# Performance work log

Measured on AMD Instinct MI355X. Metric: run time of the kernel, lower is better.

The kernel has to match this reference:

```python
import jax, jax.numpy as jnp
import numpy as np

N = 100000      # num_edges in original graph = nodes here
E = 1600000     # edges of the line-graph
F_IN = 16       # num_edge_features
H, C = 2, 32    # heads, hidden_channels
HC = H * C
TD = 16         # time_embedding_dim
CD = 16         # condition_dim
NC = 2          # num_classes
MAX_TIME = 1000.0
THETA = 1.0


def _glorot(key, shape):
    fan_in = shape[0]
    return jax.random.normal(key, shape, dtype=jnp.float32) / np.sqrt(fan_in)


def setup_inputs() -> dict:
    key = jax.random.key(0)
    ks = jax.random.split(key, 32)
    inp = {
        "x": jax.random.normal(ks[0], (N, F_IN), dtype=jnp.float32),
        "edge_index": jax.random.randint(ks[1], (2, E), 0, N, dtype=jnp.int64),
        "t": jax.random.randint(ks[2], (1,), 0, 1000, dtype=jnp.int64),
        "condition": jax.random.normal(ks[3], (N, CD), dtype=jnp.float32),
        # GATv2 layer 0 (bias=True)
        "Wl0": _glorot(ks[4], (F_IN, HC)), "bl0": jnp.zeros((HC,), jnp.float32),
        "Wr0": _glorot(ks[5], (F_IN, HC)), "br0": jnp.zeros((HC,), jnp.float32),
        "att0": _glorot(ks[6], (H, C)), "bias0": jnp.zeros((HC,), jnp.float32),
        "Wres0": _glorot(ks[7], (F_IN, HC)), "bres0": jnp.zeros((HC,), jnp.float32),
        # GATv2 layer 1 (bias=False)
        "Wl1": _glorot(ks[8], (HC, HC)),
        "Wr1": _glorot(ks[9], (HC, HC)),
        "att1": _glorot(ks[10], (H, C)),
        "Wres1": _glorot(ks[11], (HC, HC)), "bres1": jnp.zeros((HC,), jnp.float32),
        # time MLP
        "Wt0": _glorot(ks[12], (TD, TD)), "bt0": jnp.zeros((TD,), jnp.float32),
        "Wt1": _glorot(ks[13], (TD, TD)), "bt1": jnp.zeros((TD,), jnp.float32),
        # decoder heads
        "Wfd": _glorot(ks[14], (HC + CD + TD, C)), "bfd": jnp.zeros((C,), jnp.float32),
        "Wcls": _glorot(ks[15], (C, NC)), "bcls": jnp.zeros((NC,), jnp.float32),
    }
    return inp


def _segment_softmax(logits, seg, num_seg):
    # logits: [E, H], softmax over edges sharing the same destination node
    m = jax.ops.segment_max(logits, seg, num_segments=num_seg)
    ex = jnp.exp(logits - m[seg])
    s = jax.ops.segment_sum(ex, seg, num_segments=num_seg)
    return ex / (s[seg] + 1e-16)


def _gatv2(x, src, dst, Wl, bl, Wr, br, att, bias):
    # PyG GATv2Conv with add_self_loops (self loops appended by caller)
    xl = x @ Wl
    xr = x @ Wr
    if bl is not None:
        xl = xl + bl
        xr = xr + br
    xl = xl.reshape(-1, H, C)
    xr = xr.reshape(-1, H, C)
    e = jax.nn.leaky_relu(xl[src] + xr[dst], negative_slope=0.2)  # [E, H, C]
    logits = jnp.einsum('ehc,hc->eh', e, att)                     # [E, H]
    alpha = _segment_softmax(logits, dst, N)                      # [E, H]
    msg = xl[src] * alpha[:, :, None]                             # [E, H, C]
    out = jax.ops.segment_sum(msg, dst, num_segments=N)           # [N, H, C]
    out = out.reshape(N, HC)
    if bias is not None:
        out = out + bias
    return out


def _time_embedding(t):
    tf = t.astype(jnp.float32) * (1000.0 / MAX_TIME)
    half = TD // 2
    freqs = jnp.exp(jnp.arange(half, dtype=jnp.float32) * -(jnp.log(10000.0) / (half - 1)))
    ang = tf[:, None] * freqs[None, :]
    return jnp.concatenate([jnp.sin(ang), jnp.cos(ang)], axis=1)  # [1, TD]


def reference(x, edge_index, t, condition,
              Wl0, bl0, Wr0, br0, att0, bias0, Wres0, bres0,
              Wl1, Wr1, att1, Wres1, bres1,
              Wt0, bt0, Wt1, bt1, Wfd, bfd, Wcls, bcls):
    loops = jnp.arange(N, dtype=edge_index.dtype)
    src = jnp.concatenate([edge_index[0], loops])
    dst = jnp.concatenate([edge_index[1], loops])

    # layer 0
    res = jax.nn.relu(x @ Wres0 + bres0)
    h = jax.nn.relu(_gatv2(x, src, dst, Wl0, bl0, Wr0, br0, att0, bias0))
    h = THETA * h + res
    # layer 1 (bias=False)
    res = jax.nn.relu(h @ Wres1 + bres1)
    h2 = jax.nn.relu(_gatv2(h, src, dst, Wl1, None, Wr1, None, att1, None))
    h = THETA * h2 + res

    # mode == 'future'
    t_emb = _time_embedding(t)
    t_emb = jax.nn.silu(t_emb @ Wt0 + bt0)
    t_emb = jax.nn.silu(t_emb @ Wt1 + bt1)
    t_rep = jnp.tile(t_emb, (N, 1))                                # [N, TD]
    h = jnp.concatenate([h, t_rep, condition], axis=1)             # [N, HC+TD+CD]
    logits = h @ Wfd + bfd
    logits = logits @ Wcls + bcls
    return logits[None]                                            # [1, N, NC]
```

## Files before the change

kernel.cpp:

```cpp
#include <hip/hip_runtime.h>
#include <hip/hip_bf16.h>
#include <hip/hip_fp16.h>
#include <math.h>


#define BLK 256
#define BDST 32
#define CDST 256
#define CHUNK 4096
#define FCAP 768
#define NBC_MAX 512

typedef _Float16 half4v __attribute__((ext_vector_type(4)));
typedef _Float16 half2v __attribute__((ext_vector_type(2)));

#if __has_builtin(__builtin_amdgcn_fdot2)
#define FDOT2(a, b, c) __builtin_amdgcn_fdot2((a), (b), (c), false)
#else
__device__ __forceinline__ float fdot2_fallback(half2v a, half2v b, float c) {
    return c + (float)a.x * (float)b.x + (float)a.y * (float)b.y;
}
#define FDOT2(a, b, c) fdot2_fallback((a), (b), (c))
#endif

__device__ __forceinline__ float relu(float x) { return x > 0.f ? x : 0.f; }

__device__ __forceinline__ float edot(half4v h, half2v xlo, half2v xhi,
                                      half2v alo, half2v ahi, half2v c02) {
    half2v lo = half2v{h.x, h.y} + xlo;
    half2v hi = half2v{h.z, h.w} + xhi;
    lo = __builtin_elementwise_max(lo, lo * c02);
    hi = __builtin_elementwise_max(hi, hi * c02);
    return FDOT2(lo, alo, FDOT2(hi, ahi, 0.f));
}

__global__ void k_tiny(const int* __restrict__ t,
                       const float* __restrict__ Wt0, const float* __restrict__ bt0,
                       const float* __restrict__ Wt1, const float* __restrict__ bt1,
                       const float* __restrict__ Wfd, const float* __restrict__ bfd,
                       const float* __restrict__ Wcls, const float* __restrict__ bcls,
                       const float* __restrict__ Wl1, const float* __restrict__ Wr1,
                       const float* __restrict__ Wres1,
                       float* __restrict__ wcomb,
                       float* __restrict__ bfinal,
                       half4v* __restrict__ w16,
                       int* __restrict__ ccnt, int NBC)
{
    __shared__ float temb[16];
    int tid = threadIdx.x;
    for (int i = tid; i < NBC; i += BLK) ccnt[i] = 0;
    for (int idx = tid; idx < 3 * 1024; idx += BLK) {
        int m = idx >> 10, rem = idx & 1023;
        int k4 = rem >> 6, c = rem & 63;
        const float* W = (m == 0) ? Wl1 : (m == 1) ? Wr1 : Wres1;
        half4v v;
        v.x = (_Float16)W[(4 * k4 + 0) * 64 + c];
        v.y = (_Float16)W[(4 * k4 + 1) * 64 + c];
        v.z = (_Float16)W[(4 * k4 + 2) * 64 + c];
        v.w = (_Float16)W[(4 * k4 + 3) * 64 + c];
        w16[idx] = v;
    }
    if (tid == 0) {
        float tf = (float)t[0];
        float e0[16], v1[16];
        const float cexp = -logf(10000.f) / 7.f;
        for (int j = 0; j < 8; ++j) {
            float ang = tf * expf((float)j * cexp);
            e0[j] = sinf(ang);
            e0[8 + j] = cosf(ang);
        }
        for (int i = 0; i < 16; ++i) {
            float a = bt0[i];
            for (int j = 0; j < 16; ++j) a += e0[j] * Wt0[j * 16 + i];
            v1[i] = a / (1.f + expf(-a));
        }
        for (int i = 0; i < 16; ++i) {
            float a = bt1[i];
            for (int j = 0; j < 16; ++j) a += v1[j] * Wt1[j * 16 + i];
            temb[i] = a / (1.f + expf(-a));
        }
    }
    __syncthreads();
    if (tid < 192) {
        int i = tid >> 1, k = tid & 1;
        float a = 0.f;
        for (int j = 0; j < 32; ++j) a += Wfd[i * 32 + j] * Wcls[j * 2 + k];
        wcomb[tid] = a;
    }
    __syncthreads();
    if (tid < 2) {
        float a = bcls[tid];
        for (int j = 0; j < 32; ++j) a += bfd[j] * Wcls[j * 2 + tid];
        for (int d = 0; d < 16; ++d) a += temb[d] * wcomb[(64 + d) * 2 + tid];
        bfinal[tid] = a;
    }
}

__global__ void k_histc(const int* __restrict__ ei, int E, int NBC,
                        int* __restrict__ ccnt)
{
    __shared__ int h[NBC_MAX];
    int tid = threadIdx.x;
    for (int i = tid; i < NBC; i += BLK) h[i] = 0;
    __syncthreads();
    int e0 = blockIdx.x * CHUNK;
    #pragma unroll
    for (int k = 0; k < CHUNK / BLK; ++k) {
        int e = e0 + tid + k * BLK;
        if (e < E) atomicAdd(&h[ei[E + e] >> 8], 1);
    }
    __syncthreads();
    for (int i = tid; i < NBC; i += BLK) {
        int v = h[i];
        if (v) atomicAdd(&ccnt[i], v);
    }
}

__global__ void k_scan(const int* __restrict__ ccnt, int NBC, int E,
                       int* __restrict__ cbase, int* __restrict__ ccur)
{
    if (threadIdx.x == 0) {
        int acc = 0;
        for (int i = 0; i < NBC; ++i) {
            cbase[i] = acc;
            acc += ccnt[i];
        }
        cbase[NBC] = acc;
    }
    __syncthreads();
    for (int i = threadIdx.x; i < NBC; i += BLK) ccur[i] = cbase[i];
}

__global__ void k_part(const int* __restrict__ ei, int E, int NBC,
                       int* __restrict__ ccur, int* __restrict__ part)
{
    __shared__ int h[NBC_MAX];
    __shared__ int gb[NBC_MAX];
    int tid = threadIdx.x;
    int e0 = blockIdx.x * CHUNK;
    for (int i = tid; i < NBC; i += BLK) h[i] = 0;
    __syncthreads();
    int sv[CHUNK / BLK], dv[CHUNK / BLK];
    #pragma unroll
    for (int k = 0; k < CHUNK / BLK; ++k) {
        int e = e0 + tid + k * BLK;
        if (e < E) {
            sv[k] = ei[e];
            dv[k] = ei[E + e];
            atomicAdd(&h[dv[k] >> 8], 1);
        } else dv[k] = -1;
    }
    __syncthreads();
    for (int i = tid; i < NBC; i += BLK) {
        int v = h[i];
        gb[i] = v ? atomicAdd(&ccur[i], v) : 0;
    }
    __syncthreads();
    for (int i = tid; i < NBC; i += BLK) h[i] = gb[i];
    __syncthreads();
    #pragma unroll
    for (int k = 0; k < CHUNK / BLK; ++k) {
        if (dv[k] >= 0) {
            int p = atomicAdd(&h[dv[k] >> 8], 1);
            part[p] = (sv[k] << 8) | (dv[k] & 255);
        }
    }
}

__global__ void k_refine(const int* __restrict__ cbase, const int* __restrict__ part,
                         int NBF, int* __restrict__ fbeg, int* __restrict__ fend,
                         int* __restrict__ srcs)
{
    __shared__ int fcnt[8];
    __shared__ int fcur[8];
    int b = blockIdx.x, tid = threadIdx.x;
    int beg = cbase[b], end = cbase[b + 1];
    if (tid < 8) fcnt[tid] = 0;
    __syncthreads();
    for (int k = beg + tid; k < end; k += BLK)
        atomicAdd(&fcnt[(part[k] >> 5) & 7], 1);
    __syncthreads();
    if (tid == 0) {
        int acc = beg;
        #pragma unroll
        for (int f = 0; f < 8; ++f) {
            int fb = b * 8 + f;
            fcur[f] = acc;
            if (fb < NBF) { fbeg[fb] = acc; acc += fcnt[f]; fend[fb] = acc; }
        }
    }
    __syncthreads();
    for (int k = beg + tid; k < end; k += BLK) {
        int tg = part[k];
        int p = atomicAdd(&fcur[(tg >> 5) & 7], 1);
        srcs[p] = ((tg >> 8) << 5) | (tg & 31);
    }
}

__global__ void k_pre0f(const float* __restrict__ x,
                        const float* __restrict__ Wl, const float* __restrict__ bl,
                        const float* __restrict__ Wr, const float* __restrict__ br,
                        const float* __restrict__ Wres, const float* __restrict__ bres,
                        _Float16* __restrict__ xlh, _Float16* __restrict__ xr16,
                        _Float16* __restrict__ res16, int N)
{
    int wid = (int)(((long long)blockIdx.x * BLK + threadIdx.x) >> 6);
    int lane = threadIdx.x & 63;
    int g = lane >> 4, q = lane & 15;
    int n = wid * 4 + g;
    bool valid = n < N;
    int nn = valid ? n : N - 1;
    float xv = x[(size_t)nn * 16 + q];
    int c0 = q * 4;
    float4 accl = *(const float4*)(bl + c0);
    float4 accr = *(const float4*)(br + c0);
    float4 accs = *(const float4*)(bres + c0);
    #pragma unroll
    for (int k = 0; k < 16; ++k) {
        float xk = __shfl(xv, (g << 4) | k, 64);
        float4 wl = *(const float4*)(Wl + k * 64 + c0);
        float4 wr = *(const float4*)(Wr + k * 64 + c0);
        float4 wsv = *(const float4*)(Wres + k * 64 + c0);
        accl.x = fmaf(xk, wl.x, accl.x);
        accl.y = fmaf(xk, wl.y, accl.y);
        accl.z = fmaf(xk, wl.z, accl.z);
        accl.w = fmaf(xk, wl.w, accl.w);
        accr.x = fmaf(xk, wr.x, accr.x);
        accr.y = fmaf(xk, wr.y, accr.y);
        accr.z = fmaf(xk, wr.z, accr.z);
        accr.w = fmaf(xk, wr.w, accr.w);
        accs.x = fmaf(xk, wsv.x, accs.x);
        accs.y = fmaf(xk, wsv.y, accs.y);
        accs.z = fmaf(xk, wsv.z, accs.z);
        accs.w = fmaf(xk, wsv.w, accs.w);
    }
    if (valid) {
        size_t base = (size_t)n * 64 + c0;
        half4v hl, hr, hs;
        hl.x = (_Float16)accl.x; hl.y = (_Float16)accl.y;
        hl.z = (_Float16)accl.z; hl.w = (_Float16)accl.w;
        hr.x = (_Float16)accr.x; hr.y = (_Float16)accr.y;
        hr.z = (_Float16)accr.z; hr.w = (_Float16)accr.w;
        hs.x = (_Float16)relu(accs.x); hs.y = (_Float16)relu(accs.y);
        hs.z = (_Float16)relu(accs.z); hs.w = (_Float16)relu(accs.w);
        *(half4v*)(xlh + base) = hl;
        *(half4v*)(xr16 + base) = hr;
        *(half4v*)(res16 + base) = hs;
    }
}

template <int LAYER>
__global__ void k_gat3(const int* __restrict__ fbeg, const int* __restrict__ fend,
                       const int* __restrict__ srcs,
                       const _Float16* __restrict__ xlh, const _Float16* __restrict__ xr16,
                       const float* __restrict__ att, const float* __restrict__ bias,
                       const _Float16* __restrict__ res16,
                       const half4v* __restrict__ w16, const float* __restrict__ bres1,
                       _Float16* __restrict__ xlh_out, _Float16* __restrict__ xr_out,
                       _Float16* __restrict__ res_out,
                       const float* __restrict__ cond, const float* __restrict__ wcomb,
                       const float* __restrict__ bfinal, float* __restrict__ out,
                       int N)
{
    __shared__ int lh[BDST];
    __shared__ int rp[BDST + 1];
    __shared__ int cc[BDST];
    __shared__ int sidx[BDST];
    __shared__ int tags[FCAP];
    __shared__ half4v h4[LAYER == 0 ? 32 : 1][16];

    int b = blockIdx.x;
    int tid = threadIdx.x;
    int beg = fbeg[b];
    int nE = fend[b] - beg; if (nE > FCAP) nE = FCAP;

    if (tid < BDST) lh[tid] = 0;
    __syncthreads();
    for (int k = tid; k < nE; k += BLK) atomicAdd(&lh[srcs[beg + k] & 31], 1);
    __syncthreads();
    if (tid == 0) {
        int acc = 0;
        rp[0] = 0;
        #pragma unroll
        for (int i = 0; i < BDST; ++i) { acc += lh[i]; rp[i + 1] = acc; }
    }
    __syncthreads();
    if (tid < BDST) cc[tid] = rp[tid];
    __syncthreads();
    for (int k = tid; k < nE; k += BLK) {
        int tg = srcs[beg + k];
        int r = atomicAdd(&cc[tg & 31], 1);
        tags[r] = tg >> 5;
    }
    if (tid < BDST) {
        int di = rp[tid + 1] - rp[tid];
        int r = 0;
        #pragma unroll
        for (int j = 0; j < BDST; ++j) {
            int dj = rp[j + 1] - rp[j];
            r += (dj > di) || (dj == di && j < tid);
        }
        sidx[r] = tid;
    }
    __syncthreads();

    int lane = tid & 63, w = tid >> 6;
    int g = lane >> 4, q = lane & 15;
    int c0 = q * 4;
    float4 a4f = *(const float4*)(att + c0);
    const half2v c02 = { (_Float16)0.2f, (_Float16)0.2f };
    half2v alo = { (_Float16)a4f.x, (_Float16)a4f.y };
    half2v ahi = { (_Float16)a4f.z, (_Float16)a4f.w };

    #pragma unroll
    for (int rep = 0; rep < 2; ++rep) {
        int dlow = sidx[w * 8 + rep * 4 + g];
        int node = b * BDST + dlow;
        bool nvalid = node < N;
        int n = nvalid ? node : 0;

        half4v xrh = *(const half4v*)(xr16 + (size_t)n * 64 + c0);
        half2v xlo = { xrh.x, xrh.y }, xhi = { xrh.z, xrh.w };

        half4v hsv = *(const half4v*)(xlh + (size_t)n * 64 + c0);
        float lv = edot(hsv, xlo, xhi, alo, ahi, c02);
        lv += __shfl_xor(lv, 1, 8);
        lv += __shfl_xor(lv, 2, 8);
        lv += __shfl_xor(lv, 4, 8);

        float m = lv, den = 1.f;
        float ac0 = (float)hsv.x, ac1 = (float)hsv.y;
        float ac2 = (float)hsv.z, ac3 = (float)hsv.w;

        int deg = nvalid ? (rp[dlow + 1] - rp[dlow]) : 0;
        int base = nvalid ? rp[dlow] : 0;

        int t1 = max(deg, __shfl_xor(deg, 16, 64));
        int wavemax = max(t1, __shfl_xor(t1, 32, 64));

        int i1 = (0 < deg) ? tags[base + 0] : n;
        int i2 = (1 < deg) ? tags[base + 1] : n;
        int i3 = (2 < deg) ? tags[base + 2] : n;
        int i4 = (3 < deg) ? tags[base + 3] : n;
        half4v p1 = *(const half4v*)(xlh + (size_t)i1 * 64 + c0);
        half4v p2 = *(const half4v*)(xlh + (size_t)i2 * 64 + c0);
        half4v p3 = *(const half4v*)(xlh + (size_t)i3 * 64 + c0);
        half4v p4 = *(const half4v*)(xlh + (size_t)i4 * 64 + c0);

        for (int j = 0; j < wavemax; j += 4) {
            bool a1 = j < deg, a2 = j + 1 < deg, a3 = j + 2 < deg, a4b = j + 3 < deg;
            half4v h1 = p1, h2 = p2, h3 = p3, h4x = p4;
            int n1 = (j + 4 < deg) ? tags[base + j + 4] : n;
            int n2 = (j + 5 < deg) ? tags[base + j + 5] : n;
            int n3 = (j + 6 < deg) ? tags[base + j + 6] : n;
            int n4 = (j + 7 < deg) ? tags[base + j + 7] : n;
            p1 = *(const half4v*)(xlh + (size_t)n1 * 64 + c0);
            p2 = *(const half4v*)(xlh + (size_t)n2 * 64 + c0);
            p3 = *(const half4v*)(xlh + (size_t)n3 * 64 + c0);
            p4 = *(const half4v*)(xlh + (size_t)n4 * 64 + c0);

            float e1 = edot(h1, xlo, xhi, alo, ahi, c02);
            float e2 = edot(h2, xlo, xhi, alo, ahi, c02);
            float e3 = edot(h3, xlo, xhi, alo, ahi, c02);
            float e4 = edot(h4x, xlo, xhi, alo, ahi, c02);
            e1 += __shfl_xor(e1, 1, 8); e2 += __shfl_xor(e2, 1, 8);
            e3 += __shfl_xor(e3, 1, 8); e4 += __shfl_xor(e4, 1, 8);
            e1 += __shfl_xor(e1, 2, 8); e2 += __shfl_xor(e2, 2, 8);
            e3 += __shfl_xor(e3, 2, 8); e4 += __shfl_xor(e4, 2, 8);
            e1 += __shfl_xor(e1, 4, 8); e2 += __shfl_xor(e2, 4, 8);
            e3 += __shfl_xor(e3, 4, 8); e4 += __shfl_xor(e4, 4, 8);
            if (!a1) e1 = -1e30f;
            if (!a2) e2 = -1e30f;
            if (!a3) e3 = -1e30f;
            if (!a4b) e4 = -1e30f;

            float mn = fmaxf(fmaxf(m, fmaxf(e1, e2)), fmaxf(e3, e4));
            float sc  = __expf(m - mn);
            float ex1 = __expf(e1 - mn);
            float ex2 = __expf(e2 - mn);
            float ex3 = __expf(e3 - mn);
            float ex4 = __expf(e4 - mn);
            den = den * sc + ((ex1 + ex2) + (ex3 + ex4));
            ac0 = fmaf(ex4, (float)h4x.x, fmaf(ex3, (float)h3.x,
                  fmaf(ex2, (float)h2.x, fmaf(ex1, (float)h1.x, ac0 * sc))));
            ac1 = fmaf(ex4, (float)h4x.y, fmaf(ex3, (float)h3.y,
                  fmaf(ex2, (float)h2.y, fmaf(ex1, (float)h1.y, ac1 * sc))));
            ac2 = fmaf(ex4, (float)h4x.z, fmaf(ex3, (float)h3.z,
                  fmaf(ex2, (float)h2.z, fmaf(ex1, (float)h1.z, ac2 * sc))));
            ac3 = fmaf(ex4, (float)h4x.w, fmaf(ex3, (float)h3.w,
                  fmaf(ex2, (float)h2.w, fmaf(ex1, (float)h1.w, ac3 * sc))));
            m = mn;
        }

        float inv = 1.f / den;
        half4v rh = *(const half4v*)(res16 + (size_t)n * 64 + c0);
        float h0, h1, h2, h3;
        if (bias) {
            const float4 b4 = *(const float4*)(bias + c0);
            h0 = relu(ac0 * inv + b4.x) + (float)rh.x;
            h1 = relu(ac1 * inv + b4.y) + (float)rh.y;
            h2 = relu(ac2 * inv + b4.z) + (float)rh.z;
            h3 = relu(ac3 * inv + b4.w) + (float)rh.w;
        } else {
            h0 = relu(ac0 * inv) + (float)rh.x;
            h1 = relu(ac1 * inv) + (float)rh.y;
            h2 = relu(ac2 * inv) + (float)rh.z;
            h3 = relu(ac3 * inv) + (float)rh.w;
        }

        if constexpr (LAYER == 0) {
            half4v o;
            o.x = (_Float16)h0; o.y = (_Float16)h1;
            o.z = (_Float16)h2; o.w = (_Float16)h3;
            h4[dlow][q] = o;
        } else {
            float p0 = h0 * wcomb[(c0 + 0) * 2] + h1 * wcomb[(c0 + 1) * 2]
                     + h2 * wcomb[(c0 + 2) * 2] + h3 * wcomb[(c0 + 3) * 2];
            float p1d = h0 * wcomb[(c0 + 0) * 2 + 1] + h1 * wcomb[(c0 + 1) * 2 + 1]
                      + h2 * wcomb[(c0 + 2) * 2 + 1] + h3 * wcomb[(c0 + 3) * 2 + 1];
            if (q < 4) {
                float4 c4 = *(const float4*)(cond + (size_t)n * 16 + q * 4);
                int d0 = 80 + q * 4;
                p0 += c4.x * wcomb[(d0 + 0) * 2] + c4.y * wcomb[(d0 + 1) * 2]
                    + c4.z * wcomb[(d0 + 2) * 2] + c4.w * wcomb[(d0 + 3) * 2];
                p1d += c4.x * wcomb[(d0 + 0) * 2 + 1] + c4.y * wcomb[(d0 + 1) * 2 + 1]
                     + c4.z * wcomb[(d0 + 2) * 2 + 1] + c4.w * wcomb[(d0 + 3) * 2 + 1];
            }
            #pragma unroll
            for (int off = 1; off < 16; off <<= 1) {
                p0 += __shfl_xor(p0, off, 16);
                p1d += __shfl_xor(p1d, off, 16);
            }
            if (q == 0 && nvalid) {
                out[(size_t)n * 2] = p0 + bfinal[0];
                out[(size_t)n * 2 + 1] = p1d + bfinal[1];
            }
        }
    }

    if constexpr (LAYER == 0) {
        __syncthreads();
        int nb = b * BDST;
        int c = tid & 63, ww = tid >> 6;
        float al[8], ar[8], as2[8];
        float vbs = bres1[c];
        #pragma unroll
        for (int i = 0; i < 8; ++i) { al[i] = 0.f; ar[i] = 0.f; as2[i] = vbs; }

        #pragma unroll 4
        for (int k4 = 0; k4 < 16; ++k4) {
            half4v wl = w16[k4 * 64 + c];
            half4v wr = w16[1024 + k4 * 64 + c];
            half4v wsv = w16[2048 + k4 * 64 + c];
            half2v wll = { wl.x, wl.y },  wlh = { wl.z, wl.w };
            half2v wrl = { wr.x, wr.y },  wrh = { wr.z, wr.w };
            half2v wsl = { wsv.x, wsv.y }, wsh = { wsv.z, wsv.w };
            #pragma unroll
            for (int i = 0; i < 8; ++i) {
                half4v hv = h4[ww * 8 + i][k4];
                half2v hl = { hv.x, hv.y }, hh = { hv.z, hv.w };
                al[i] = FDOT2(hl, wll, al[i]);
                al[i] = FDOT2(hh, wlh, al[i]);
                ar[i] = FDOT2(hl, wrl, ar[i]);
                ar[i] = FDOT2(hh, wrh, ar[i]);
                as2[i] = FDOT2(hl, wsl, as2[i]);
                as2[i] = FDOT2(hh, wsh, as2[i]);
            }
        }
        #pragma unroll
        for (int i = 0; i < 8; ++i) {
            int n = nb + ww * 8 + i;
            if (n < N) {
                xlh_out[(size_t)n * 64 + c] = (_Float16)al[i];
                xr_out[(size_t)n * 64 + c]  = (_Float16)ar[i];
                res_out[(size_t)n * 64 + c] = (_Float16)relu(as2[i]);
            }
        }
    }
}

static inline int gblk(long long threads) { return (int)((threads + BLK - 1) / BLK); }

extern "C" void kernel_launch(void* const* d_in, const int* in_sizes, int n_in,
                              void* d_out, int out_size, void* d_ws, size_t ws_size,
                              hipStream_t stream) {
    const float* x     = (const float*)d_in[0];
    const int*   ei    = (const int*)d_in[1];
    const int*   t     = (const int*)d_in[2];
    const float* cond  = (const float*)d_in[3];
    const float* Wl0   = (const float*)d_in[4];
    const float* bl0   = (const float*)d_in[5];
    const float* Wr0   = (const float*)d_in[6];
    const float* br0   = (const float*)d_in[7];
    const float* att0  = (const float*)d_in[8];
    const float* bias0 = (const float*)d_in[9];
    const float* Wres0 = (const float*)d_in[10];
    const float* bres0 = (const float*)d_in[11];
    const float* Wl1   = (const float*)d_in[12];
    const float* Wr1   = (const float*)d_in[13];
    const float* att1  = (const float*)d_in[14];
    const float* Wres1 = (const float*)d_in[15];
    const float* bres1 = (const float*)d_in[16];
    const float* Wt0   = (const float*)d_in[17];
    const float* bt0   = (const float*)d_in[18];
    const float* Wt1   = (const float*)d_in[19];
    const float* bt1   = (const float*)d_in[20];
    const float* Wfd   = (const float*)d_in[21];
    const float* bfd   = (const float*)d_in[22];
    const float* Wcls  = (const float*)d_in[23];
    const float* bcls  = (const float*)d_in[24];
    float* out = (float*)d_out;

    const int N   = in_sizes[0] / 16;
    const int E   = in_sizes[1] / 2;
    const int NBC = (N + CDST - 1) / CDST;
    const int NBF = (N + BDST - 1) / BDST;

    float* ws = (float*)d_ws;
    size_t o = 0;
    _Float16* xlhA  = (_Float16*)(ws + o); o += (size_t)N * 32;
    _Float16* xlhB  = (_Float16*)(ws + o); o += (size_t)N * 32;
    _Float16* xr16  = (_Float16*)(ws + o); o += (size_t)N * 32;
    _Float16* res16 = (_Float16*)(ws + o); o += (size_t)N * 32;
    half4v* w16  = (half4v*)(ws + o); o += 3 * 1024 * 2;
    float* wcomb = ws + o; o += 192;
    float* bfin  = ws + o; o += 2;
    int* iws     = (int*)(ws + o);
    size_t io = 0;
    int* ccnt  = iws + io; io += NBC_MAX;
    int* cbase = iws + io; io += NBC_MAX + 1;
    int* ccur  = iws + io; io += NBC_MAX;
    int* fbeg  = iws + io; io += NBF;
    int* fend  = iws + io; io += NBF;
    int* part  = iws + io; io += E;
    int* srcs  = iws + io; io += E;

    const int partBlocks = (E + CHUNK - 1) / CHUNK;

    k_tiny<<<1, BLK, 0, stream>>>(t, Wt0, bt0, Wt1, bt1, Wfd, bfd, Wcls, bcls,
                                  Wl1, Wr1, Wres1, wcomb, bfin, w16, ccnt, NBC);

    k_histc<<<partBlocks, BLK, 0, stream>>>(ei, E, NBC, ccnt);
    k_scan<<<1, BLK, 0, stream>>>(ccnt, NBC, E, cbase, ccur);
    k_part<<<partBlocks, BLK, 0, stream>>>(ei, E, NBC, ccur, part);
    k_refine<<<NBC, BLK, 0, stream>>>(cbase, part, NBF, fbeg, fend, srcs);

    k_pre0f<<<gblk((long long)((N + 3) / 4) * 64), BLK, 0, stream>>>(
        x, Wl0, bl0, Wr0, br0, Wres0, bres0, xlhA, xr16, res16, N);

    k_gat3<0><<<NBF, BLK, 0, stream>>>(fbeg, fend, srcs, xlhA, xr16, att0, bias0, res16,
                                       w16, bres1, xlhB, xr16, res16,
                                       nullptr, nullptr, nullptr, nullptr, N);

    k_gat3<1><<<NBF, BLK, 0, stream>>>(fbeg, fend, srcs, xlhB, xr16, att1, nullptr, res16,
                                       nullptr, nullptr, nullptr, nullptr, nullptr,
                                       cond, wcomb, bfin, out, N);
}
```

Baseline: 272.9 us.

## Build full CSR rowptr in refine and fold scan into histogram kernel

The refine pass now bins edges per destination node (256 bins per coarse bucket) and writes a full CSR rowptr, so both GAT kernels just load contiguous sorted sources instead of re-sorting each 32-node block's edges in shared memory. The separate single-thread scan kernel is removed; the last histogram block, detected with an atomic done counter, computes the prefix sums. FCAP is raised to 1024 and degrees are clamped to the cap. The cost is a serial 256-step loop per refine block, more shared atomics there, and a last-block-done pattern whose correctness depends on fence ordering.

```diff
diff --git a/kernel.cpp b/kernel.cpp
--- a/kernel.cpp
+++ b/kernel.cpp
@@ -8,7 +8,7 @@
 #define BDST 32
 #define CDST 256
 #define CHUNK 4096
-#define FCAP 768
+#define FCAP 1024
 #define NBC_MAX 512
 
 typedef _Float16 half4v __attribute__((ext_vector_type(4)));
@@ -44,11 +44,12 @@
                        float* __restrict__ wcomb,
                        float* __restrict__ bfinal,
                        half4v* __restrict__ w16,
-                       int* __restrict__ ccnt, int NBC)
+                       int* __restrict__ ccnt, int* __restrict__ donecnt, int NBC)
 {
     __shared__ float temb[16];
     int tid = threadIdx.x;
     for (int i = tid; i < NBC; i += BLK) ccnt[i] = 0;
+    if (tid == 0) *donecnt = 0;
     for (int idx = tid; idx < 3 * 1024; idx += BLK) {
         int m = idx >> 10, rem = idx & 1023;
         int k4 = rem >> 6, c = rem & 63;
@@ -97,9 +98,12 @@
 }
 
 __global__ void k_histc(const int* __restrict__ ei, int E, int NBC,
-                        int* __restrict__ ccnt)
+                        int* __restrict__ ccnt, int* __restrict__ donecnt,
+                        int* __restrict__ cbase, int* __restrict__ ccur,
+                        int nblocks)
 {
     __shared__ int h[NBC_MAX];
+    __shared__ int amlast;
     int tid = threadIdx.x;
     for (int i = tid; i < NBC; i += BLK) h[i] = 0;
     __syncthreads();
@@ -114,21 +118,21 @@
         int v = h[i];
         if (v) atomicAdd(&ccnt[i], v);
     }
-}
-
-__global__ void k_scan(const int* __restrict__ ccnt, int NBC, int E,
-                       int* __restrict__ cbase, int* __restrict__ ccur)
-{
-    if (threadIdx.x == 0) {
-        int acc = 0;
-        for (int i = 0; i < NBC; ++i) {
-            cbase[i] = acc;
-            acc += ccnt[i];
-        }
-        cbase[NBC] = acc;
-    }
-    __syncthreads();
-    for (int i = threadIdx.x; i < NBC; i += BLK) ccur[i] = cbase[i];
+    __threadfence();
+    if (tid == 0) amlast = (atomicAdd(donecnt, 1) == nblocks - 1) ? 1 : 0;
+    __syncthreads();
+    if (amlast) {
+        for (int i = tid; i < NBC; i += BLK)
+            h[i] = atomicAdd(&ccnt[i], 0);
+        __syncthreads();
+        if (tid == 0) {
+            int acc = 0;
+            for (int i = 0; i < NBC; ++i) { cbase[i] = acc; acc += h[i]; }
+            cbase[NBC] = acc;
+        }
+        __syncthreads();
+        for (int i = tid; i < NBC; i += BLK) ccur[i] = cbase[i];
+    }
 }
 
 __global__ void k_part(const int* __restrict__ ei, int E, int NBC,
@@ -168,32 +172,33 @@
 }
 
 __global__ void k_refine(const int* __restrict__ cbase, const int* __restrict__ part,
-                         int NBF, int* __restrict__ fbeg, int* __restrict__ fend,
-                         int* __restrict__ srcs)
+                         int N, int* __restrict__ rowptr, int* __restrict__ srcs)
 {
-    __shared__ int fcnt[8];
-    __shared__ int fcur[8];
+    __shared__ int fcnt[CDST];
+    __shared__ int fcur[CDST];
     int b = blockIdx.x, tid = threadIdx.x;
     int beg = cbase[b], end = cbase[b + 1];
-    if (tid < 8) fcnt[tid] = 0;
+    fcnt[tid] = 0;
     __syncthreads();
     for (int k = beg + tid; k < end; k += BLK)
-        atomicAdd(&fcnt[(part[k] >> 5) & 7], 1);
+        atomicAdd(&fcnt[part[k] & 255], 1);
     __syncthreads();
     if (tid == 0) {
         int acc = beg;
-        #pragma unroll
-        for (int f = 0; f < 8; ++f) {
-            int fb = b * 8 + f;
-            fcur[f] = acc;
-            if (fb < NBF) { fbeg[fb] = acc; acc += fcnt[f]; fend[fb] = acc; }
-        }
+        #pragma unroll 8
+        for (int i = 0; i < CDST; ++i) {
+            fcur[i] = acc;
+            int nd = b * CDST + i;
+            if (nd < N) rowptr[nd] = acc;
+            acc += fcnt[i];
+        }
+        if (b == gridDim.x - 1) rowptr[N] = acc;
     }
     __syncthreads();
     for (int k = beg + tid; k < end; k += BLK) {
         int tg = part[k];
-        int p = atomicAdd(&fcur[(tg >> 5) & 7], 1);
-        srcs[p] = ((tg >> 8) << 5) | (tg & 31);
+        int p = atomicAdd(&fcur[tg & 255], 1);
+        srcs[p] = tg >> 8;
     }
 }
 
@@ -250,7 +255,7 @@
 }
 
 template <int LAYER>
-__global__ void k_gat3(const int* __restrict__ fbeg, const int* __restrict__ fend,
+__global__ void k_gat3(const int* __restrict__ rowptr,
                        const int* __restrict__ srcs,
                        const _Float16* __restrict__ xlh, const _Float16* __restrict__ xr16,
                        const float* __restrict__ att, const float* __restrict__ bias,
@@ -262,36 +267,23 @@
                        const float* __restrict__ bfinal, float* __restrict__ out,
                        int N)
 {
-    __shared__ int lh[BDST];
     __shared__ int rp[BDST + 1];
-    __shared__ int cc[BDST];
     __shared__ int sidx[BDST];
     __shared__ int tags[FCAP];
     __shared__ half4v h4[LAYER == 0 ? 32 : 1][16];
 
     int b = blockIdx.x;
     int tid = threadIdx.x;
-    int beg = fbeg[b];
-    int nE = fend[b] - beg; if (nE > FCAP) nE = FCAP;
-
-    if (tid < BDST) lh[tid] = 0;
-    __syncthreads();
-    for (int k = tid; k < nE; k += BLK) atomicAdd(&lh[srcs[beg + k] & 31], 1);
-    __syncthreads();
-    if (tid == 0) {
-        int acc = 0;
-        rp[0] = 0;
-        #pragma unroll
-        for (int i = 0; i < BDST; ++i) { acc += lh[i]; rp[i + 1] = acc; }
-    }
-    __syncthreads();
-    if (tid < BDST) cc[tid] = rp[tid];
-    __syncthreads();
-    for (int k = tid; k < nE; k += BLK) {
-        int tg = srcs[beg + k];
-        int r = atomicAdd(&cc[tg & 31], 1);
-        tags[r] = tg >> 5;
-    }
+    int nb = b * BDST;
+
+    if (tid < BDST + 1) {
+        int nd = nb + tid; if (nd > N) nd = N;
+        rp[tid] = rowptr[nd];
+    }
+    __syncthreads();
+    int beg = rp[0];
+    int nE = rp[BDST] - beg; if (nE > FCAP) nE = FCAP;
+    for (int k = tid; k < nE; k += BLK) tags[k] = srcs[beg + k];
     if (tid < BDST) {
         int di = rp[tid + 1] - rp[tid];
         int r = 0;
@@ -315,7 +307,7 @@
     #pragma unroll
     for (int rep = 0; rep < 2; ++rep) {
         int dlow = sidx[w * 8 + rep * 4 + g];
-        int node = b * BDST + dlow;
+        int node = nb + dlow;
         bool nvalid = node < N;
         int n = nvalid ? node : 0;
 
@@ -333,7 +325,8 @@
         float ac2 = (float)hsv.z, ac3 = (float)hsv.w;
 
         int deg = nvalid ? (rp[dlow + 1] - rp[dlow]) : 0;
-        int base = nvalid ? rp[dlow] : 0;
+        int base = nvalid ? (rp[dlow] - beg) : 0;
+        if (base + deg > nE) deg = (base < nE) ? nE - base : 0;
 
         int t1 = max(deg, __shfl_xor(deg, 16, 64));
         int wavemax = max(t1, __shfl_xor(t1, 32, 64));
@@ -440,7 +433,6 @@
 
     if constexpr (LAYER == 0) {
         __syncthreads();
-        int nb = b * BDST;
         int c = tid & 63, ww = tid >> 6;
         float al[8], ar[8], as2[8];
         float vbs = bres1[c];
@@ -527,32 +519,31 @@
     float* bfin  = ws + o; o += 2;
     int* iws     = (int*)(ws + o);
     size_t io = 0;
-    int* ccnt  = iws + io; io += NBC_MAX;
-    int* cbase = iws + io; io += NBC_MAX + 1;
-    int* ccur  = iws + io; io += NBC_MAX;
-    int* fbeg  = iws + io; io += NBF;
-    int* fend  = iws + io; io += NBF;
-    int* part  = iws + io; io += E;
-    int* srcs  = iws + io; io += E;
+    int* ccnt    = iws + io; io += NBC_MAX;
+    int* cbase   = iws + io; io += NBC_MAX + 1;
+    int* ccur    = iws + io; io += NBC_MAX;
+    int* donecnt = iws + io; io += 1;
+    int* rowptr  = iws + io; io += (size_t)N + 1;
+    int* part    = iws + io; io += E;
+    int* srcs    = iws + io; io += E;
 
     const int partBlocks = (E + CHUNK - 1) / CHUNK;
 
     k_tiny<<<1, BLK, 0, stream>>>(t, Wt0, bt0, Wt1, bt1, Wfd, bfd, Wcls, bcls,
-                                  Wl1, Wr1, Wres1, wcomb, bfin, w16, ccnt, NBC);
-
-    k_histc<<<partBlocks, BLK, 0, stream>>>(ei, E, NBC, ccnt);
-    k_scan<<<1, BLK, 0, stream>>>(ccnt, NBC, E, cbase, ccur);
+                                  Wl1, Wr1, Wres1, wcomb, bfin, w16, ccnt, donecnt, NBC);
+
+    k_histc<<<partBlocks, BLK, 0, stream>>>(ei, E, NBC, ccnt, donecnt, cbase, ccur, partBlocks);
     k_part<<<partBlocks, BLK, 0, stream>>>(ei, E, NBC, ccur, part);
-    k_refine<<<NBC, BLK, 0, stream>>>(cbase, part, NBF, fbeg, fend, srcs);
+    k_refine<<<NBC, BLK, 0, stream>>>(cbase, part, N, rowptr, srcs);
 
     k_pre0f<<<gblk((long long)((N + 3) / 4) * 64), BLK, 0, stream>>>(
         x, Wl0, bl0, Wr0, br0, Wres0, bres0, xlhA, xr16, res16, N);
 
-    k_gat3<0><<<NBF, BLK, 0, stream>>>(fbeg, fend, srcs, xlhA, xr16, att0, bias0, res16,
+    k_gat3<0><<<NBF, BLK, 0, stream>>>(rowptr, srcs, xlhA, xr16, att0, bias0, res16,
                                        w16, bres1, xlhB, xr16, res16,
                                        nullptr, nullptr, nullptr, nullptr, N);
 
-    k_gat3<1><<<NBF, BLK, 0, stream>>>(fbeg, fend, srcs, xlhB, xr16, att1, nullptr, res16,
+    k_gat3<1><<<NBF, BLK, 0, stream>>>(rowptr, srcs, xlhB, xr16, att1, nullptr, res16,
                                        nullptr, nullptr, nullptr, nullptr, nullptr,
                                        cond, wcomb, bfin, out, N);
 }
```

Measured after the change: 283.3 us. +3.8%, slower.
